# Kernel optimization log

Measured on AMD Instinct MI355X. Metric: run time of the kernel, lower is better.

## Reference

```python
import jax, jax.numpy as jnp
import numpy as np

D = 64        # input_dim (also per-head dim)
H = 8         # num_heads
L = 128       # split_length (block size)
NEG = -1e9


def _causal_mask(n):
    # additive causal mask: 0 on/below diagonal, -1e9 above
    i = jnp.arange(n)
    return jnp.where(i[:, None] >= i[None, :], 0.0, NEG).astype(jnp.float32)


def setup_inputs() -> dict:
    key = jax.random.key(0)
    ks = jax.random.split(key, 11)
    B, S = 4, 8192
    s = 1.0 / np.sqrt(D)
    inp = {
        "Q": jax.random.normal(ks[0], (B, S, D), jnp.float32),
        "K": jax.random.normal(ks[1], (B, S, D), jnp.float32),
        "V": jax.random.normal(ks[2], (B, S, D), jnp.float32),
        "WQ_w": jax.random.normal(ks[3], (H * D, D), jnp.float32) * s,
        "WQ_b": jnp.zeros((H * D,), jnp.float32),
        "WK_w": jax.random.normal(ks[4], (H * D, D), jnp.float32) * s,
        "WK_b": jnp.zeros((H * D,), jnp.float32),
        "WV_w": jax.random.normal(ks[5], (H * D, D), jnp.float32) * s,
        "WV_b": jnp.zeros((H * D,), jnp.float32),
        "W_w": jax.random.normal(ks[6], (D, H * D), jnp.float32) * (1.0 / np.sqrt(H * D)),
        "W_b": jnp.zeros((D,), jnp.float32),
    }
    return inp


def reference(Q, K, V, WQ_w, WQ_b, WK_w, WK_b, WV_w, WV_b, W_w, W_b):
    B, S, _ = Q.shape
    n = S // L  # number of blocks
    scale = 1.0 / jnp.sqrt(jnp.float32(D))

    def split(x, w, b):
        y = x @ w.T + b                              # [B,S,H*D]
        y = y.reshape(B, n, L, H, D)
        return y.transpose(0, 1, 3, 2, 4)            # [B,n,H,L,D]

    rQ = split(Q, WQ_w, WQ_b)
    rK = split(K, WK_w, WK_b)
    rV = split(V, WV_w, WV_b)

    # block-local causal attention
    s_mask = _causal_mask(L)
    Si = jnp.einsum('bnhqd,bnhkd->bnhqk', rQ, rK) * scale + s_mask
    sim = jax.nn.softmax(Si, axis=-1)
    oV = jnp.einsum('bnhqk,bnhkd->bnhqd', sim, rV)   # [B,n,H,L,D]

    # pooled global attention over blocks
    pooling = oV.mean(axis=3).transpose(0, 2, 1, 3)  # [B,H,n,D]
    g_mask = _causal_mask(n)
    g_Si = jnp.einsum('bhqd,bhkd->bhqk', pooling, pooling) * scale + g_mask
    g_sim = jax.nn.softmax(g_Si, axis=-1)
    global_att = jnp.einsum('bhqk,bhkd->bhqd', g_sim, pooling)  # [B,H,n,D]
    global_att = global_att.transpose(0, 2, 1, 3)    # [B,n,H,D]

    # broadcast-add global context to every position in the block
    oV = oV + global_att[:, :, :, None, :]           # [B,n,H,L,D]

    # merge heads then output projection
    merged = oV.transpose(0, 1, 3, 2, 4).reshape(B, S, H * D)
    out = merged @ W_w.T + W_b                       # [B,S,D]
    return out
```

## Files before the change

### kernel.cpp

```cpp
#include <hip/hip_runtime.h>
#include <stdint.h>

typedef float  v4f  __attribute__((ext_vector_type(4)));
typedef __bf16 v8bf __attribute__((ext_vector_type(8)));
typedef __bf16 v4bf __attribute__((ext_vector_type(4)));
typedef unsigned short u16;

#define NEGBIG (-1.0e9f)

static __device__ __forceinline__ uint2 pack4(v4f a){
  v4bf r;
  r[0]=(__bf16)a[0]; r[1]=(__bf16)a[1]; r[2]=(__bf16)a[2]; r[3]=(__bf16)a[3];
  return __builtin_bit_cast(uint2, r);
}
static __device__ __forceinline__ v8bf pack8(float4 a, float4 b){
  v8bf r;
  r[0]=(__bf16)a.x; r[1]=(__bf16)a.y; r[2]=(__bf16)a.z; r[3]=(__bf16)a.w;
  r[4]=(__bf16)b.x; r[5]=(__bf16)b.y; r[6]=(__bf16)b.z; r[7]=(__bf16)b.w;
  return r;
}
static __device__ __forceinline__ v4f mfma16(v8bf a, v8bf b, v4f c){
  return __builtin_amdgcn_mfma_f32_16x16x32_bf16(a, b, c, 0, 0, 0);
}

static __device__ __forceinline__ v8bf bfly(uint2 t0, uint2 t1, int srcA, int srcB, int hi){
  int a0 = __shfl((int)t0.x, srcA), a1 = __shfl((int)t0.y, srcA);
  int b0 = __shfl((int)t1.x, srcA), b1 = __shfl((int)t1.y, srcA);
  int a2 = __shfl((int)t0.x, srcB), a3 = __shfl((int)t0.y, srcB);
  int b2 = __shfl((int)t1.x, srcB), b3 = __shfl((int)t1.y, srcB);
  uint4 r;
  r.x = hi ? (unsigned)b0 : (unsigned)a0;
  r.y = hi ? (unsigned)b1 : (unsigned)a1;
  r.z = hi ? (unsigned)b2 : (unsigned)a2;
  r.w = hi ? (unsigned)b3 : (unsigned)a3;
  return __builtin_bit_cast(v8bf, r);
}

__global__ __launch_bounds__(256) void k_pre(
    const float* __restrict__ WQ, const float* __restrict__ WK,
    const float* __restrict__ WV, const float* __restrict__ Ww,
    u16* __restrict__ wq, u16* __restrict__ wk,
    u16* __restrict__ wv, u16* __restrict__ ww)
{
  const int seg = blockIdx.x >> 5;
  const int idx = ((blockIdx.x & 31)*256 + threadIdx.x)*4;
  const float* s = (seg==0) ? WQ : (seg==1) ? WK : (seg==2) ? WV : Ww;
  u16*       dst = (seg==0) ? wq : (seg==1) ? wk : (seg==2) ? wv : ww;
  float4 v = *(const float4*)(s + idx);
  v4f a; a[0]=v.x; a[1]=v.y; a[2]=v.z; a[3]=v.w;
  *(uint2*)(dst + idx) = pack4(a);
}

#define LDS_RK    0
#define LDS_VT    16384
#define LDS_WS    32768
#define LDS_POOL  57344
#define LDS_TOTAL 61440

__global__ __launch_bounds__(512, 4) void k_fused(
    const float* __restrict__ Q, const float* __restrict__ K, const float* __restrict__ V,
    const u16* __restrict__ wqbf, const u16* __restrict__ wkbf,
    const u16* __restrict__ wvbf, const u16* __restrict__ wwbf,
    const float* __restrict__ bQ, const float* __restrict__ bK, const float* __restrict__ bV,
    float* __restrict__ oVW, float* __restrict__ pool)
{
  __shared__ char lds[LDS_TOTAL];

  const int bid = blockIdx.x;
  const int hg  = bid & 1;
  const int tile = bid >> 1;
  const int b = tile >> 6, nb = tile & 63;
  const int rowbase = tile * 128;
  const int tid = threadIdx.x;
  const int w = tid >> 6, l = tid & 63;
  const int l15 = l & 15, g = l >> 4;
  const int swz = (l15 & 7) << 4;
  const int srcA = ((l >> 4) & 1) * 32 + l15;
  const int srcB = srcA + 16;
  const int hi_  = l >> 5;
  const float scale = 0.125f;

  auto STAGE = [&](int hn){
    #pragma unroll
    for (int i = 0; i < 3; ++i){
      const int obase = w*3072 + i*1024;
      const int m   = obase >> 13;
      const int row = ((obase & 8191) >> 7) + (l >> 3);
      const int sc  = (l & 7) << 4;
      const u16* basep = (m == 0) ? wqbf : (m == 1) ? wkbf : wvbf;
      const char* src = (const char*)basep + hn*8192 + row*128 + (sc ^ ((row & 7) << 4));
      __builtin_amdgcn_global_load_lds(
          (const __attribute__((address_space(1))) unsigned int*)src,
          (__attribute__((address_space(3))) unsigned int*)(lds + LDS_WS + obase),
          16, 0, 0);
    }
  };

  STAGE(hg*4);

  const int xrow = rowbase + w*16 + l15;
  v8bf xq[2], xk[2], xv[2];
  #pragma unroll
  for (int ks = 0; ks < 2; ++ks){
    const float* qp = Q + xrow*64 + ks*32 + g*8;
    const float* kp = K + xrow*64 + ks*32 + g*8;
    const float* vp = V + xrow*64 + ks*32 + g*8;
    xq[ks] = pack8(*(const float4*)qp, *(const float4*)(qp+4));
    xk[ks] = pack8(*(const float4*)kp, *(const float4*)(kp+4));
    xv[ks] = pack8(*(const float4*)vp, *(const float4*)(vp+4));
  }

  __syncthreads();

  v4f acc_out[4];
  #pragma unroll
  for (int mt = 0; mt < 4; ++mt){ v4f z = {0.f,0.f,0.f,0.f}; acc_out[mt] = z; }

  const int q = w*16 + l15;

  for (int hi = 0; hi < 4; ++hi){
    const int h  = hg*4 + hi;
    const int hb = h*64;
    char* wsb = lds + LDS_WS;

    v4f aq[4], ak[4];
    #pragma unroll
    for (int mt = 0; mt < 4; ++mt){
      float4 b4 = *(const float4*)(bQ + hb + mt*16 + g*4);
      aq[mt][0]=b4.x; aq[mt][1]=b4.y; aq[mt][2]=b4.z; aq[mt][3]=b4.w;
      float4 c4 = *(const float4*)(bK + hb + mt*16 + g*4);
      ak[mt][0]=c4.x; ak[mt][1]=c4.y; ak[mt][2]=c4.z; ak[mt][3]=c4.w;
    }
    #pragma unroll
    for (int ks = 0; ks < 2; ++ks){
      #pragma unroll
      for (int mt = 0; mt < 4; ++mt){
        v8bf wqf = *(const v8bf*)(wsb + (mt*16 + l15)*128 + ((ks*64 + g*16) ^ swz));
        aq[mt] = mfma16(wqf, xq[ks], aq[mt]);
      }
      #pragma unroll
      for (int mt = 0; mt < 4; ++mt){
        v8bf wkf = *(const v8bf*)(wsb + 8192 + (mt*16 + l15)*128 + ((ks*64 + g*16) ^ swz));
        ak[mt] = mfma16(wkf, xk[ks], ak[mt]);
      }
    }
    uint2 pq[4];
    #pragma unroll
    for (int mt = 0; mt < 4; ++mt) pq[mt] = pack4(aq[mt]);
    v8bf qf0 = bfly(pq[0], pq[1], srcA, srcB, hi_);
    v8bf qf1 = bfly(pq[2], pq[3], srcA, srcB, hi_);
    #pragma unroll
    for (int mt = 0; mt < 4; ++mt)
      *(uint2*)(lds + LDS_RK + (w*16 + l15)*128 + ((mt*32 + g*8) ^ swz)) = pack4(ak[mt]);

    {
      v4f av[4];
      #pragma unroll
      for (int nt = 0; nt < 4; ++nt){
        float bs = bV[hb + nt*16 + l15];
        av[nt][0]=bs; av[nt][1]=bs; av[nt][2]=bs; av[nt][3]=bs;
      }
      #pragma unroll
      for (int ks = 0; ks < 2; ++ks)
        #pragma unroll
        for (int nt = 0; nt < 4; ++nt){
          v8bf wvf = *(const v8bf*)(wsb + 16384 + (nt*16 + l15)*128 + ((ks*64 + g*16) ^ swz));
          av[nt] = mfma16(xv[ks], wvf, av[nt]);
        }
      #pragma unroll
      for (int nt = 0; nt < 4; ++nt)
        *(uint2*)(lds + LDS_VT + (nt*16 + l15)*256 + ((w*32 + g*8) ^ swz)) = pack4(av[nt]);
    }

    __syncthreads();

    if (hi < 3) STAGE(h+1);

    if (hi > 0 && tid < 64){
      const float* pr = (const float*)(lds + LDS_POOL + ((hi-1)&1)*2048);
      float s_ = 0.f;
      #pragma unroll
      for (int p = 0; p < 8; ++p) s_ += pr[p*64 + tid];
      pool[(b*8 + h-1)*4096 + nb*64 + tid] = s_ * (1.0f/128.0f);
    }

    float sum = 0.f;
    uint2 pp[8];
    __builtin_amdgcn_s_setprio(1);
    #pragma unroll
    for (int mt = 0; mt < 8; ++mt){
      if (mt > w){ uint2 z; z.x = 0u; z.y = 0u; pp[mt] = z; continue; }
      v4f s4 = {0.f,0.f,0.f,0.f};
      s4 = mfma16(*(const v8bf*)(lds + LDS_RK + (mt*16 + l15)*128 + ((0*64 + g*16) ^ swz)), qf0, s4);
      s4 = mfma16(*(const v8bf*)(lds + LDS_RK + (mt*16 + l15)*128 + ((1*64 + g*16) ^ swz)), qf1, s4);
      v4f e4;
      #pragma unroll
      for (int r = 0; r < 4; ++r){
        const int key = mt*16 + g*4 + r;
        float v_ = (key <= q) ? s4[r]*scale : NEGBIG;
        float p = __expf(v_);
        e4[r] = p;
        sum += p;
      }
      pp[mt] = pack4(e4);
    }
    __builtin_amdgcn_s_setprio(0);
    sum += __shfl_xor(sum, 16);
    sum += __shfl_xor(sum, 32);
    const float inv = 1.0f / sum;

    v4f oa[4];
    #pragma unroll
    for (int mt = 0; mt < 4; ++mt){ v4f z = {0.f,0.f,0.f,0.f}; oa[mt] = z; }
    const int WKn = (w >> 1) + 1;
    __builtin_amdgcn_s_setprio(1);
    #pragma unroll
    for (int ks = 0; ks < 4; ++ks){
      if (ks >= WKn) continue;
      v8bf pf = bfly(pp[2*ks], pp[2*ks+1], srcA, srcB, hi_);
      #pragma unroll
      for (int mt = 0; mt < 4; ++mt){
        v8bf vf = *(const v8bf*)(lds + LDS_VT + (mt*16 + l15)*256 + ((ks*64 + g*16) ^ swz));
        oa[mt] = mfma16(vf, pf, oa[mt]);
      }
    }
    __builtin_amdgcn_s_setprio(0);

    #pragma unroll
    for (int mt = 0; mt < 4; ++mt){
      oa[mt][0]*=inv; oa[mt][1]*=inv; oa[mt][2]*=inv; oa[mt][3]*=inv;
    }

    {
      float* prd = (float*)(lds + LDS_POOL + (hi&1)*2048);
      #pragma unroll
      for (int mt = 0; mt < 4; ++mt){
        v4f v = oa[mt];
        #pragma unroll
        for (int s_ = 1; s_ < 16; s_ <<= 1){
          v[0] += __shfl_xor(v[0], s_);
          v[1] += __shfl_xor(v[1], s_);
          v[2] += __shfl_xor(v[2], s_);
          v[3] += __shfl_xor(v[3], s_);
        }
        if (l15 == 0)
          *(float4*)(prd + w*64 + mt*16 + g*4) = make_float4(v[0], v[1], v[2], v[3]);
      }
    }

    uint2 po[4];
    #pragma unroll
    for (int mt = 0; mt < 4; ++mt) po[mt] = pack4(oa[mt]);
    v8bf of0 = bfly(po[0], po[1], srcA, srcB, hi_);
    v8bf of1 = bfly(po[2], po[3], srcA, srcB, hi_);
    #pragma unroll
    for (int ks = 0; ks < 2; ++ks){
      v8bf off = ks ? of1 : of0;
      #pragma unroll
      for (int mt = 0; mt < 4; ++mt){
        v8bf wf = *(const v8bf*)(wwbf + (mt*16 + l15)*512 + hb + ks*32 + g*8);
        acc_out[mt] = mfma16(wf, off, acc_out[mt]);
      }
    }

    __syncthreads();
  }

  if (tid < 64){
    const float* pr = (const float*)(lds + LDS_POOL + (3&1)*2048);
    float s_ = 0.f;
    #pragma unroll
    for (int p = 0; p < 8; ++p) s_ += pr[p*64 + tid];
    pool[(b*8 + hg*4 + 3)*4096 + nb*64 + tid] = s_ * (1.0f/128.0f);
  }

  #pragma unroll
  for (int mt = 0; mt < 4; ++mt){
    float4 o;
    o.x = acc_out[mt][0]; o.y = acc_out[mt][1];
    o.z = acc_out[mt][2]; o.w = acc_out[mt][3];
    *(float4*)(oVW + hg*2097152 + (rowbase + w*16 + l15)*64 + mt*16 + g*4) = o;
  }
}

__global__ __launch_bounds__(256) void k_global(
    const float* __restrict__ pool, float* __restrict__ gatt)
{
  __shared__ float pl[64*68];
  __shared__ float pm[64*68];

  const int bid = blockIdx.x;
  const int tid = threadIdx.x;

  const int base = bid * 4096;
  for (int e = tid; e < 4096; e += 256)
    pl[(e >> 6)*68 + (e & 63)] = pool[base + e];
  __syncthreads();

  const int r = tid >> 2, qq = tid & 3;

  float rowv[64];
  #pragma unroll
  for (int dd = 0; dd < 16; ++dd){
    float4 t = *(const float4*)(&pl[r*68 + dd*4]);
    rowv[dd*4+0] = t.x; rowv[dd*4+1] = t.y; rowv[dd*4+2] = t.z; rowv[dd*4+3] = t.w;
  }

  float sv[16];
  #pragma unroll
  for (int cc = 0; cc < 16; ++cc){
    const int c = qq*16 + cc;
    float dot = 0.f;
    #pragma unroll
    for (int dd = 0; dd < 16; ++dd){
      float4 t = *(const float4*)(&pl[c*68 + dd*4]);
      dot += t.x*rowv[dd*4+0] + t.y*rowv[dd*4+1] + t.z*rowv[dd*4+2] + t.w*rowv[dd*4+3];
    }
    sv[cc] = (c <= r) ? dot*0.125f : NEGBIG;
  }
  float mx = -3.0e38f;
  #pragma unroll
  for (int cc = 0; cc < 16; ++cc) mx = fmaxf(mx, sv[cc]);
  mx = fmaxf(mx, __shfl_xor(mx, 1));
  mx = fmaxf(mx, __shfl_xor(mx, 2));
  float sum = 0.f;
  #pragma unroll
  for (int cc = 0; cc < 16; ++cc){ float p = __expf(sv[cc] - mx); sv[cc] = p; sum += p; }
  sum += __shfl_xor(sum, 1);
  sum += __shfl_xor(sum, 2);
  const float inv = 1.0f / sum;
  #pragma unroll
  for (int cc = 0; cc < 16; ++cc) pm[r*68 + qq*16 + cc] = sv[cc]*inv;
  __syncthreads();

  float acc[16];
  #pragma unroll
  for (int i = 0; i < 16; ++i) acc[i] = 0.f;
  for (int c = 0; c < 64; ++c){
    const float pv = pm[r*68 + c];
    const float* row = &pl[c*68 + qq*16];
    float4 t0 = *(const float4*)(row + 0);
    float4 t1 = *(const float4*)(row + 4);
    float4 t2 = *(const float4*)(row + 8);
    float4 t3 = *(const float4*)(row + 12);
    acc[0]  += pv*t0.x; acc[1]  += pv*t0.y; acc[2]  += pv*t0.z; acc[3]  += pv*t0.w;
    acc[4]  += pv*t1.x; acc[5]  += pv*t1.y; acc[6]  += pv*t1.z; acc[7]  += pv*t1.w;
    acc[8]  += pv*t2.x; acc[9]  += pv*t2.y; acc[10] += pv*t2.z; acc[11] += pv*t2.w;
    acc[12] += pv*t3.x; acc[13] += pv*t3.y; acc[14] += pv*t3.z; acc[15] += pv*t3.w;
  }
  #pragma unroll
  for (int dd = 0; dd < 4; ++dd){
    float4 o;
    o.x = acc[dd*4+0]; o.y = acc[dd*4+1]; o.z = acc[dd*4+2]; o.w = acc[dd*4+3];
    *(float4*)(&gatt[base + r*64 + qq*16 + dd*4]) = o;
  }
}

__global__ __launch_bounds__(512) void k_final(
    const float* __restrict__ oVW, const float* __restrict__ Ww, const float* __restrict__ Wb,
    const float* __restrict__ gatt, float* __restrict__ out)
{
  __shared__ float gred[8][64];
  __shared__ float gadd[64];

  const int bid = blockIdx.x;
  const int b = bid >> 6, nb = bid & 63;
  const int rowbase = bid * 128;
  const int tid = threadIdx.x;

  {
    const int dout = tid & 63;
    const int h = tid >> 6;
    const float* gr = gatt + (b*8 + h)*4096 + nb*64;
    const float* wr = Ww + dout*512 + h*64;
    float a = 0.f;
    #pragma unroll
    for (int dd = 0; dd < 16; ++dd){
      float4 g4 = *(const float4*)(gr + dd*4);
      float4 w4 = *(const float4*)(wr + dd*4);
      a += g4.x*w4.x + g4.y*w4.y + g4.z*w4.z + g4.w*w4.w;
    }
    gred[h][dout] = a;
  }
  __syncthreads();
  if (tid < 64){
    float s = Wb[tid];
    #pragma unroll
    for (int p = 0; p < 8; ++p) s += gred[p][tid];
    gadd[tid] = s;
  }
  __syncthreads();

  const int c4 = (tid & 15) * 4;
  float4 ga = *(const float4*)(&gadd[c4]);
  #pragma unroll
  for (int it = 0; it < 4; ++it){
    const int row = it*32 + (tid >> 4);
    float4 v0 = *(const float4*)(oVW + (rowbase + row)*64 + c4);
    float4 v1 = *(const float4*)(oVW + 2097152 + (rowbase + row)*64 + c4);
    float4 o;
    o.x = v0.x + v1.x + ga.x; o.y = v0.y + v1.y + ga.y;
    o.z = v0.z + v1.z + ga.z; o.w = v0.w + v1.w + ga.w;
    *(float4*)(out + (rowbase + row)*64 + c4) = o;
  }
}


extern "C" void kernel_launch(void* const* d_in, const int* in_sizes, int n_in,
                              void* d_out, int out_size, void* d_ws, size_t ws_size,
                              hipStream_t stream) {
  const float* Q   = (const float*)d_in[0];
  const float* K   = (const float*)d_in[1];
  const float* V   = (const float*)d_in[2];
  const float* WQw = (const float*)d_in[3];
  const float* WQb = (const float*)d_in[4];
  const float* WKw = (const float*)d_in[5];
  const float* WKb = (const float*)d_in[6];
  const float* WVw = (const float*)d_in[7];
  const float* WVb = (const float*)d_in[8];
  const float* Ww  = (const float*)d_in[9];
  const float* Wb  = (const float*)d_in[10];

  char* ws = (char*)d_ws;
  float* oVW  = (float*)(ws + 0);
  float* pool = (float*)(ws + 16777216);
  float* gatt = (float*)(ws + 17301504);
  u16*   wqbf = (u16*)(ws + 17825792);
  u16*   wkbf = (u16*)(ws + 17891328);
  u16*   wvbf = (u16*)(ws + 17956864);
  u16*   wwbf = (u16*)(ws + 18022400);

  float* outp = (float*)d_out;

  k_pre<<<128, 256, 0, stream>>>(WQw, WKw, WVw, Ww, wqbf, wkbf, wvbf, wwbf);
  k_fused<<<512, 512, 0, stream>>>(Q, K, V, wqbf, wkbf, wvbf, wwbf,
                                   WQb, WKb, WVb, oVW, pool);
  k_global<<<32, 256, 0, stream>>>(pool, gatt);
  k_final<<<256, 512, 0, stream>>>(oVW, Ww, Wb, gatt, outp);
}
```

Baseline: 91.49 us.

## Read projection weights directly from global memory instead of staging through LDS

Removes the async global-to-LDS staging of the per-head Q/K/V bf16 weight slices and has each lane load its MFMA weight fragments straight from global (L2/L1-cached) memory. This cuts LDS usage from about 60KB to 36KB and raises the launch-bounds occupancy hint from 4 to 8 blocks. The trade-off is more global/L1 traffic and load latency on the critical MFMA path, and it drops the prefetch overlap for the next head's weights.

```diff
diff --git a/kernel.cpp b/kernel.cpp
--- a/kernel.cpp
+++ b/kernel.cpp
@@ -53,11 +53,10 @@
 
 #define LDS_RK    0
 #define LDS_VT    16384
-#define LDS_WS    32768
-#define LDS_POOL  57344
-#define LDS_TOTAL 61440
-
-__global__ __launch_bounds__(512, 4) void k_fused(
+#define LDS_POOL  32768
+#define LDS_TOTAL 36864
+
+__global__ __launch_bounds__(512, 8) void k_fused(
     const float* __restrict__ Q, const float* __restrict__ K, const float* __restrict__ V,
     const u16* __restrict__ wqbf, const u16* __restrict__ wkbf,
     const u16* __restrict__ wvbf, const u16* __restrict__ wwbf,
@@ -80,24 +79,6 @@
   const int hi_  = l >> 5;
   const float scale = 0.125f;
 
-  auto STAGE = [&](int hn){
-    #pragma unroll
-    for (int i = 0; i < 3; ++i){
-      const int obase = w*3072 + i*1024;
-      const int m   = obase >> 13;
-      const int row = ((obase & 8191) >> 7) + (l >> 3);
-      const int sc  = (l & 7) << 4;
-      const u16* basep = (m == 0) ? wqbf : (m == 1) ? wkbf : wvbf;
-      const char* src = (const char*)basep + hn*8192 + row*128 + (sc ^ ((row & 7) << 4));
-      __builtin_amdgcn_global_load_lds(
-          (const __attribute__((address_space(1))) unsigned int*)src,
-          (__attribute__((address_space(3))) unsigned int*)(lds + LDS_WS + obase),
-          16, 0, 0);
-    }
-  };
-
-  STAGE(hg*4);
-
   const int xrow = rowbase + w*16 + l15;
   v8bf xq[2], xk[2], xv[2];
   #pragma unroll
@@ -110,18 +91,19 @@
     xv[ks] = pack8(*(const float4*)vp, *(const float4*)(vp+4));
   }
 
-  __syncthreads();
-
   v4f acc_out[4];
   #pragma unroll
   for (int mt = 0; mt < 4; ++mt){ v4f z = {0.f,0.f,0.f,0.f}; acc_out[mt] = z; }
 
   const int q = w*16 + l15;
+  const int wfo = l15*64 + g*8;
 
   for (int hi = 0; hi < 4; ++hi){
     const int h  = hg*4 + hi;
     const int hb = h*64;
-    char* wsb = lds + LDS_WS;
+    const u16* wqp = wqbf + hb*64 + wfo;
+    const u16* wkp = wkbf + hb*64 + wfo;
+    const u16* wvp = wvbf + hb*64 + wfo;
 
     v4f aq[4], ak[4];
     #pragma unroll
@@ -135,12 +117,12 @@
     for (int ks = 0; ks < 2; ++ks){
       #pragma unroll
       for (int mt = 0; mt < 4; ++mt){
-        v8bf wqf = *(const v8bf*)(wsb + (mt*16 + l15)*128 + ((ks*64 + g*16) ^ swz));
+        v8bf wqf = *(const v8bf*)(wqp + mt*1024 + ks*32);
         aq[mt] = mfma16(wqf, xq[ks], aq[mt]);
       }
       #pragma unroll
       for (int mt = 0; mt < 4; ++mt){
-        v8bf wkf = *(const v8bf*)(wsb + 8192 + (mt*16 + l15)*128 + ((ks*64 + g*16) ^ swz));
+        v8bf wkf = *(const v8bf*)(wkp + mt*1024 + ks*32);
         ak[mt] = mfma16(wkf, xk[ks], ak[mt]);
       }
     }
@@ -164,7 +146,7 @@
       for (int ks = 0; ks < 2; ++ks)
         #pragma unroll
         for (int nt = 0; nt < 4; ++nt){
-          v8bf wvf = *(const v8bf*)(wsb + 16384 + (nt*16 + l15)*128 + ((ks*64 + g*16) ^ swz));
+          v8bf wvf = *(const v8bf*)(wvp + nt*1024 + ks*32);
           av[nt] = mfma16(xv[ks], wvf, av[nt]);
         }
       #pragma unroll
@@ -173,8 +155,6 @@
     }
 
     __syncthreads();
-
-    if (hi < 3) STAGE(h+1);
 
     if (hi > 0 && tid < 64){
       const float* pr = (const float*)(lds + LDS_POOL + ((hi-1)&1)*2048);
```

Measured after the change: 149.3 us. 1.63x slower.

## Fuse pooled global attention into final kernel, removing separate k_global launch

Applied to the files above, without the earlier changes.

Each final-stage block now loads the pooled block summaries for all heads into shared memory and computes only its own query row of the global attention, instead of relying on a separate kernel that writes the full global-attention tensor. This removes one kernel launch and the global round trip for the intermediate buffer. In exchange, every block redundantly reads the full pool tile per head and adds several block-wide barriers. The padded stride of 65 with float4 shared accesses may produce misaligned LDS vector accesses.

```diff
diff --git a/kernel.cpp b/kernel.cpp
--- a/kernel.cpp
+++ b/kernel.cpp
@@ -283,83 +283,13 @@
   }
 }
 
-__global__ __launch_bounds__(256) void k_global(
-    const float* __restrict__ pool, float* __restrict__ gatt)
-{
-  __shared__ float pl[64*68];
-  __shared__ float pm[64*68];
-
-  const int bid = blockIdx.x;
-  const int tid = threadIdx.x;
-
-  const int base = bid * 4096;
-  for (int e = tid; e < 4096; e += 256)
-    pl[(e >> 6)*68 + (e & 63)] = pool[base + e];
-  __syncthreads();
-
-  const int r = tid >> 2, qq = tid & 3;
-
-  float rowv[64];
-  #pragma unroll
-  for (int dd = 0; dd < 16; ++dd){
-    float4 t = *(const float4*)(&pl[r*68 + dd*4]);
-    rowv[dd*4+0] = t.x; rowv[dd*4+1] = t.y; rowv[dd*4+2] = t.z; rowv[dd*4+3] = t.w;
-  }
-
-  float sv[16];
-  #pragma unroll
-  for (int cc = 0; cc < 16; ++cc){
-    const int c = qq*16 + cc;
-    float dot = 0.f;
-    #pragma unroll
-    for (int dd = 0; dd < 16; ++dd){
-      float4 t = *(const float4*)(&pl[c*68 + dd*4]);
-      dot += t.x*rowv[dd*4+0] + t.y*rowv[dd*4+1] + t.z*rowv[dd*4+2] + t.w*rowv[dd*4+3];
-    }
-    sv[cc] = (c <= r) ? dot*0.125f : NEGBIG;
-  }
-  float mx = -3.0e38f;
-  #pragma unroll
-  for (int cc = 0; cc < 16; ++cc) mx = fmaxf(mx, sv[cc]);
-  mx = fmaxf(mx, __shfl_xor(mx, 1));
-  mx = fmaxf(mx, __shfl_xor(mx, 2));
-  float sum = 0.f;
-  #pragma unroll
-  for (int cc = 0; cc < 16; ++cc){ float p = __expf(sv[cc] - mx); sv[cc] = p; sum += p; }
-  sum += __shfl_xor(sum, 1);
-  sum += __shfl_xor(sum, 2);
-  const float inv = 1.0f / sum;
-  #pragma unroll
-  for (int cc = 0; cc < 16; ++cc) pm[r*68 + qq*16 + cc] = sv[cc]*inv;
-  __syncthreads();
-
-  float acc[16];
-  #pragma unroll
-  for (int i = 0; i < 16; ++i) acc[i] = 0.f;
-  for (int c = 0; c < 64; ++c){
-    const float pv = pm[r*68 + c];
-    const float* row = &pl[c*68 + qq*16];
-    float4 t0 = *(const float4*)(row + 0);
-    float4 t1 = *(const float4*)(row + 4);
-    float4 t2 = *(const float4*)(row + 8);
-    float4 t3 = *(const float4*)(row + 12);
-    acc[0]  += pv*t0.x; acc[1]  += pv*t0.y; acc[2]  += pv*t0.z; acc[3]  += pv*t0.w;
-    acc[4]  += pv*t1.x; acc[5]  += pv*t1.y; acc[6]  += pv*t1.z; acc[7]  += pv*t1.w;
-    acc[8]  += pv*t2.x; acc[9]  += pv*t2.y; acc[10] += pv*t2.z; acc[11] += pv*t2.w;
-    acc[12] += pv*t3.x; acc[13] += pv*t3.y; acc[14] += pv*t3.z; acc[15] += pv*t3.w;
-  }
-  #pragma unroll
-  for (int dd = 0; dd < 4; ++dd){
-    float4 o;
-    o.x = acc[dd*4+0]; o.y = acc[dd*4+1]; o.z = acc[dd*4+2]; o.w = acc[dd*4+3];
-    *(float4*)(&gatt[base + r*64 + qq*16 + dd*4]) = o;
-  }
-}
-
 __global__ __launch_bounds__(512) void k_final(
     const float* __restrict__ oVW, const float* __restrict__ Ww, const float* __restrict__ Wb,
-    const float* __restrict__ gatt, float* __restrict__ out)
+    const float* __restrict__ pool, float* __restrict__ out)
 {
+  __shared__ float pl[64*65];
+  __shared__ float prow[64];
+  __shared__ float grow[8][64];
   __shared__ float gred[8][64];
   __shared__ float gadd[64];
 
@@ -368,11 +298,64 @@
   const int rowbase = bid * 128;
   const int tid = threadIdx.x;
 
+  for (int h = 0; h < 8; ++h){
+    const float* pb = pool + (b*8 + h)*4096;
+    {
+      const int e = tid*8;
+      float4 a0 = *(const float4*)(pb + e);
+      float4 a1 = *(const float4*)(pb + e + 4);
+      const int k = e >> 6, d = e & 63;
+      *(float4*)(&pl[k*65 + d])     = a0;
+      *(float4*)(&pl[k*65 + d + 4]) = a1;
+    }
+    __syncthreads();
+
+    if (tid < 64){
+      const int k = tid;
+      float dot = 0.f;
+      #pragma unroll
+      for (int dd = 0; dd < 16; ++dd){
+        float4 t  = *(const float4*)(&pl[k*65  + dd*4]);
+        float4 qv = *(const float4*)(&pl[nb*65 + dd*4]);
+        dot += t.x*qv.x + t.y*qv.y + t.z*qv.z + t.w*qv.w;
+      }
+      float sv = (k <= nb) ? dot*0.125f : NEGBIG;
+      float mx = sv;
+      #pragma unroll
+      for (int s = 1; s < 64; s <<= 1) mx = fmaxf(mx, __shfl_xor(mx, s));
+      float p = __expf(sv - mx);
+      float sum = p;
+      #pragma unroll
+      for (int s = 1; s < 64; s <<= 1) sum += __shfl_xor(sum, s);
+      prow[k] = p / sum;
+    }
+    __syncthreads();
+
+    {
+      const int d = tid & 63, kk = tid >> 6;
+      float a = 0.f;
+      #pragma unroll
+      for (int j = 0; j < 8; ++j){
+        const int k = kk*8 + j;
+        a += prow[k] * pl[k*65 + d];
+      }
+      gred[kk][d] = a;
+    }
+    __syncthreads();
+    if (tid < 64){
+      float a = 0.f;
+      #pragma unroll
+      for (int p = 0; p < 8; ++p) a += gred[p][tid];
+      grow[h][tid] = a;
+    }
+    __syncthreads();
+  }
+
   {
     const int dout = tid & 63;
     const int h = tid >> 6;
-    const float* gr = gatt + (b*8 + h)*4096 + nb*64;
     const float* wr = Ww + dout*512 + h*64;
+    const float* gr = &grow[h][0];
     float a = 0.f;
     #pragma unroll
     for (int dd = 0; dd < 16; ++dd){
@@ -396,12 +379,13 @@
   #pragma unroll
   for (int it = 0; it < 4; ++it){
     const int row = it*32 + (tid >> 4);
-    float4 v0 = *(const float4*)(oVW + (rowbase + row)*64 + c4);
-    float4 v1 = *(const float4*)(oVW + 2097152 + (rowbase + row)*64 + c4);
+    const int idx = (rowbase + row)*64 + c4;
+    float4 v0 = *(const float4*)(oVW + idx);
+    float4 v1 = *(const float4*)(oVW + 2097152 + idx);
     float4 o;
     o.x = v0.x + v1.x + ga.x; o.y = v0.y + v1.y + ga.y;
     o.z = v0.z + v1.z + ga.z; o.w = v0.w + v1.w + ga.w;
-    *(float4*)(out + (rowbase + row)*64 + c4) = o;
+    *(float4*)(out + idx) = o;
   }
 }
 
@@ -424,7 +408,6 @@
   char* ws = (char*)d_ws;
   float* oVW  = (float*)(ws + 0);
   float* pool = (float*)(ws + 16777216);
-  float* gatt = (float*)(ws + 17301504);
   u16*   wqbf = (u16*)(ws + 17825792);
   u16*   wkbf = (u16*)(ws + 17891328);
   u16*   wvbf = (u16*)(ws + 17956864);
@@ -435,6 +418,5 @@
   k_pre<<<128, 256, 0, stream>>>(WQw, WKw, WVw, Ww, wqbf, wkbf, wvbf, wwbf);
   k_fused<<<512, 512, 0, stream>>>(Q, K, V, wqbf, wkbf, wvbf, wwbf,
                                    WQb, WKb, WVb, oVW, pool);
-  k_global<<<32, 256, 0, stream>>>(pool, gatt);
-  k_final<<<256, 512, 0, stream>>>(oVW, Ww, Wb, gatt, outp);
-}
+  k_final<<<256, 512, 0, stream>>>(oVW, Ww, Wb, pool, outp);
+}
```

After: 88.89 us. -2.8%, faster.
